# Kernel tuning notes

Measured on AMD Instinct MI355X. Metric: run time of the kernel, lower is better.

The kernel has to match this reference:

```python
import jax, jax.numpy as jnp
import numpy as np

N_NODES = 100000
N_EDGES = 1600000
IN_DIM, HID_DIM, OUT_DIM = 256, 128, 64


def gcn_conv(x, row, col, w, W, b, n):
    # PyG GCNConv (eval): add self-loops (weight 1), symmetric normalization,
    # linear transform, scatter-add aggregation at target nodes.
    row = jnp.concatenate([row, jnp.arange(n, dtype=row.dtype)])
    col = jnp.concatenate([col, jnp.arange(n, dtype=col.dtype)])
    w = jnp.concatenate([w, jnp.ones((n,), dtype=w.dtype)])
    deg = jax.ops.segment_sum(w, col, num_segments=n)  # [N]
    dinv = jnp.where(deg > 0, jax.lax.rsqrt(deg), 0.0)
    norm = dinv[row] * w * dinv[col]  # [E+N]
    h = x @ W  # [N, out]
    msg = norm[:, None] * h[row]  # gather: [E+N, out]
    out = jax.ops.segment_sum(msg, col, num_segments=n)  # scatter-add
    return out + b


def setup_inputs() -> dict:
    key = jax.random.key(0)
    k = jax.random.split(key, 8)
    x = jax.random.normal(k[0], (N_NODES, IN_DIM), dtype=jnp.float32)
    edge_index = jax.random.randint(k[1], (2, N_EDGES), 0, N_NODES, dtype=jnp.int64)
    edge_weight = jax.random.uniform(k[2], (N_EDGES,), dtype=jnp.float32)
    s1 = 1.0 / np.sqrt(IN_DIM)
    s2 = 1.0 / np.sqrt(HID_DIM)
    W1 = jax.random.uniform(k[3], (IN_DIM, HID_DIM), minval=-s1, maxval=s1, dtype=jnp.float32)
    b1 = jnp.zeros((HID_DIM,), dtype=jnp.float32)
    W2 = jax.random.uniform(k[4], (HID_DIM, OUT_DIM), minval=-s2, maxval=s2, dtype=jnp.float32)
    b2 = jnp.zeros((OUT_DIM,), dtype=jnp.float32)
    return {"x": x, "edge_index": edge_index, "edge_weight": edge_weight,
            "W1": W1, "b1": b1, "W2": W2, "b2": b2}


def reference(x, edge_index, edge_weight, W1, b1, W2, b2):
    row, col = edge_index[0], edge_index[1]
    n = x.shape[0]
    h = gcn_conv(x, row, col, edge_weight, W1, b1, n)
    h = jax.nn.relu(h)  # dropout is identity in eval mode
    out = gcn_conv(h, row, col, edge_weight, W2, b2, n)
    return out
```

## Files before the change

### kernel.cpp

```cpp
#include <hip/hip_runtime.h>
#include <hip/hip_fp16.h>

#define IN_DIM 256
#define HID_DIM 128
#define OUT_DIM 64

typedef short s8v __attribute__((ext_vector_type(8)));
typedef float f32x4 __attribute__((ext_vector_type(4)));


__device__ __forceinline__ unsigned short bf16_rne(float f) {
    unsigned int u = __float_as_uint(f);
    u += 0x7FFFu + ((u >> 16) & 1u);
    return (unsigned short)(u >> 16);
}
__device__ __forceinline__ float bfbits_to_f(unsigned short h) {
    return __uint_as_float(((unsigned int)h) << 16);
}
__device__ __forceinline__ void cvt_split4(float4 f, uint2& hv, uint2& lv) {
    unsigned short h0 = bf16_rne(f.x), h1 = bf16_rne(f.y);
    unsigned short h2 = bf16_rne(f.z), h3 = bf16_rne(f.w);
    unsigned short l0 = bf16_rne(f.x - bfbits_to_f(h0));
    unsigned short l1 = bf16_rne(f.y - bfbits_to_f(h1));
    unsigned short l2 = bf16_rne(f.z - bfbits_to_f(h2));
    unsigned short l3 = bf16_rne(f.w - bfbits_to_f(h3));
    hv.x = (unsigned int)h0 | ((unsigned int)h1 << 16);
    hv.y = (unsigned int)h2 | ((unsigned int)h3 << 16);
    lv.x = (unsigned int)l0 | ((unsigned int)l1 << 16);
    lv.y = (unsigned int)l2 | ((unsigned int)l3 << 16);
}

__global__ __launch_bounds__(256) void wsplit_kernel(const float* __restrict__ W,
        unsigned short* __restrict__ wth, unsigned short* __restrict__ wtl,
        int K, int NCOL) {
    int idx = blockIdx.x * 256 + threadIdx.x;
    if (idx < K * NCOL) {
        int k = idx / NCOL, nn = idx % NCOL;
        float f = W[idx];
        unsigned short h = bf16_rne(f);
        unsigned short l = bf16_rne(f - bfbits_to_f(h));
        wth[nn * K + k] = h;
        wtl[nn * K + k] = l;
    }
}


#define FPSCALE 16777216.0f
#define FPMASK  ((1ULL << 40) - 1)

__global__ __launch_bounds__(256) void init_kernel(unsigned long long* packed, int n) {
    int i = blockIdx.x * 256 + threadIdx.x;
    if (i < n) packed[i] = (1ULL << 24);
}

__global__ __launch_bounds__(256) void deg_cnt_kernel(const int* __restrict__ col,
        const float* __restrict__ w, unsigned long long* packed, int e) {
    int i = blockIdx.x * 256 + threadIdx.x;
    if (i < e) {
        unsigned long long v = (1ULL << 40) |
            (unsigned long long)(w[i] * FPSCALE + 0.5f);
        atomicAdd(&packed[col[i]], v);
    }
}

__global__ __launch_bounds__(256) void dinv_kernel(const unsigned long long* __restrict__ packed,
        float* __restrict__ dinv, int* __restrict__ cnt, int n) {
    int i = blockIdx.x * 256 + threadIdx.x;
    if (i < n) {
        unsigned long long p = packed[i];
        float d = (float)(p & FPMASK) * (1.0f / FPSCALE);
        dinv[i] = d > 0.0f ? rsqrtf(d) : 0.0f;
        cnt[i] = (int)(p >> 40);
    }
}


__global__ __launch_bounds__(256) void scan1_kernel(const int* __restrict__ cnt,
        int* __restrict__ bsum, int n) {
    int t = threadIdx.x;
    int base = blockIdx.x * 1024 + t * 4;
    int s = 0;
    if (base + 3 < n) {
        int4 v = *(const int4*)(cnt + base);
        s = v.x + v.y + v.z + v.w;
    } else {
        for (int i = 0; i < 4; i++) if (base + i < n) s += cnt[base + i];
    }
    __shared__ int sm[256];
    sm[t] = s;
    __syncthreads();
    for (int d = 1; d < 256; d <<= 1) {
        int v = (t >= d) ? sm[t - d] : 0;
        __syncthreads();
        sm[t] += v;
        __syncthreads();
    }
    if (t == 255) bsum[blockIdx.x] = sm[255];
}

__global__ __launch_bounds__(1024) void scan2_kernel(int* bsum, int* total_out, int nb) {
    __shared__ int sm[1024];
    int t = threadIdx.x;
    int v = (t < nb) ? bsum[t] : 0;
    sm[t] = v;
    __syncthreads();
    for (int d = 1; d < 1024; d <<= 1) {
        int u = (t >= d) ? sm[t - d] : 0;
        __syncthreads();
        sm[t] += u;
        __syncthreads();
    }
    int ex = (t == 0) ? 0 : sm[t - 1];
    if (t < nb) bsum[t] = ex;
    if (t == nb - 1) *total_out = sm[t];
}

__global__ __launch_bounds__(256) void scan3_kernel(const int* __restrict__ cnt,
        const int* __restrict__ bsum, int* __restrict__ offsets,
        int* __restrict__ cursors, int n) {
    int t = threadIdx.x;
    int base = blockIdx.x * 1024 + t * 4;
    int a[4] = {0, 0, 0, 0};
    if (base + 3 < n) {
        int4 v = *(const int4*)(cnt + base);
        a[0] = v.x; a[1] = v.y; a[2] = v.z; a[3] = v.w;
    } else {
        for (int i = 0; i < 4; i++) if (base + i < n) a[i] = cnt[base + i];
    }
    int s = a[0] + a[1] + a[2] + a[3];
    __shared__ int sm[256];
    sm[t] = s;
    __syncthreads();
    for (int d = 1; d < 256; d <<= 1) {
        int u = (t >= d) ? sm[t - d] : 0;
        __syncthreads();
        sm[t] += u;
        __syncthreads();
    }
    int pre = bsum[blockIdx.x] + ((t == 0) ? 0 : sm[t - 1]);
    int o0 = pre, o1 = o0 + a[0], o2 = o1 + a[1], o3 = o2 + a[2];
    if (base + 3 < n) {
        *(int4*)(offsets + base) = make_int4(o0, o1, o2, o3);
        *(int4*)(cursors + base) = make_int4(o0, o1, o2, o3);
    } else {
        int o[4] = {o0, o1, o2, o3};
        for (int i = 0; i < 4; i++) if (base + i < n) {
            offsets[base + i] = o[i];
            cursors[base + i] = o[i];
        }
    }
}

__global__ __launch_bounds__(256) void fill_csc_kernel(const int* __restrict__ row,
        const int* __restrict__ col, const float* __restrict__ w,
        const float* __restrict__ dinv, int* cursors,
        int2* __restrict__ csc, int e) {
    int i = blockIdx.x * 256 + threadIdx.x;
    if (i < e) {
        int r = row[i], c = col[i];
        float nrm = dinv[r] * w[i] * dinv[c];
        int p = atomicAdd(&cursors[c], 1);
        csc[p] = make_int2(r, __float_as_int(nrm));
    }
}


template<int K, int NCOL>
__global__ __launch_bounds__(256) void gemm_mfma_kernel(
        const float* __restrict__ x, const unsigned short* __restrict__ wth,
        const unsigned short* __restrict__ wtl, __half* __restrict__ out, int n) {
    constexpr int NT = NCOL / 16;
    constexpr int NCH = K / 32;
    __shared__ unsigned short sAh[128 * 40];
    __shared__ unsigned short sAl[128 * 40];
    __shared__ unsigned short sBh[NCOL * 40];
    __shared__ unsigned short sBl[NCOL * 40];

    int t = threadIdx.x;
    int wave = t >> 6, lane = t & 63, quad = lane >> 4, r16 = lane & 15;
    long rowBase = (long)blockIdx.x * 128;

    f32x4 acc[2][NT];
#pragma unroll
    for (int mi = 0; mi < 2; mi++)
#pragma unroll
        for (int nt = 0; nt < NT; nt++) acc[mi][nt] = (f32x4)0.0f;

    int srow = t >> 1;
    int skseg = (t & 1) * 16;
    long sgr = rowBase + srow; if (sgr > n - 1) sgr = n - 1;
    const float* xrow = x + sgr * K + skseg;

    for (int kc = 0; kc < NCH; kc++) {
        const float4* xs = (const float4*)(xrow + kc * 32);
        float4 f0 = xs[0], f1 = xs[1], f2 = xs[2], f3 = xs[3];
        uint2 h0, l0, h1, l1, h2, l2, h3, l3;
        cvt_split4(f0, h0, l0); cvt_split4(f1, h1, l1);
        cvt_split4(f2, h2, l2); cvt_split4(f3, h3, l3);
        *(uint4*)(sAh + srow * 40 + skseg)     = make_uint4(h0.x, h0.y, h1.x, h1.y);
        *(uint4*)(sAh + srow * 40 + skseg + 8) = make_uint4(h2.x, h2.y, h3.x, h3.y);
        *(uint4*)(sAl + srow * 40 + skseg)     = make_uint4(l0.x, l0.y, l1.x, l1.y);
        *(uint4*)(sAl + srow * 40 + skseg + 8) = make_uint4(l2.x, l2.y, l3.x, l3.y);
        for (int c = t; c < NCOL * 4; c += 256) {
            int nn = c >> 2, ks = (c & 3) * 8;
            *(uint4*)(sBh + nn * 40 + ks) = *(const uint4*)(wth + nn * K + kc * 32 + ks);
            *(uint4*)(sBl + nn * 40 + ks) = *(const uint4*)(wtl + nn * K + kc * 32 + ks);
        }
        __syncthreads();
        const unsigned short* pa  = sAh + (wave * 32 + r16) * 40 + quad * 8;
        const unsigned short* pal = sAl + (wave * 32 + r16) * 40 + quad * 8;
        s8v ah0 = *(const s8v*)pa;
        s8v ah1 = *(const s8v*)(pa + 16 * 40);
        s8v al0 = *(const s8v*)pal;
        s8v al1 = *(const s8v*)(pal + 16 * 40);
#pragma unroll
        for (int nt = 0; nt < NT; nt++) {
            const unsigned short* pb  = sBh + (nt * 16 + r16) * 40 + quad * 8;
            const unsigned short* pbl = sBl + (nt * 16 + r16) * 40 + quad * 8;
            s8v bh = *(const s8v*)pb;
            s8v bl = *(const s8v*)pbl;
            acc[0][nt] = __builtin_amdgcn_mfma_f32_16x16x32_bf16(ah0, bh, acc[0][nt], 0, 0, 0);
            acc[0][nt] = __builtin_amdgcn_mfma_f32_16x16x32_bf16(al0, bh, acc[0][nt], 0, 0, 0);
            acc[0][nt] = __builtin_amdgcn_mfma_f32_16x16x32_bf16(ah0, bl, acc[0][nt], 0, 0, 0);
            acc[1][nt] = __builtin_amdgcn_mfma_f32_16x16x32_bf16(ah1, bh, acc[1][nt], 0, 0, 0);
            acc[1][nt] = __builtin_amdgcn_mfma_f32_16x16x32_bf16(al1, bh, acc[1][nt], 0, 0, 0);
            acc[1][nt] = __builtin_amdgcn_mfma_f32_16x16x32_bf16(ah1, bl, acc[1][nt], 0, 0, 0);
        }
        __syncthreads();
    }
#pragma unroll
    for (int mi = 0; mi < 2; mi++) {
        long gr0 = rowBase + wave * 32 + mi * 16 + quad * 4;
#pragma unroll
        for (int nt = 0; nt < NT; nt++) {
            f32x4 d = acc[mi][nt];
#pragma unroll
            for (int i = 0; i < 4; i++) {
                long gr = gr0 + i;
                if (gr < n) out[gr * NCOL + nt * 16 + r16] = __float2half(d[i]);
            }
        }
    }
}


__device__ __forceinline__ void acc8(float* a, uint4 raw, float w) {
    __half2* hp = (__half2*)&raw;
    float2 f0 = __half22float2(hp[0]);
    float2 f1 = __half22float2(hp[1]);
    float2 f2 = __half22float2(hp[2]);
    float2 f3 = __half22float2(hp[3]);
    a[0] += w * f0.x; a[1] += w * f0.y; a[2] += w * f1.x; a[3] += w * f1.y;
    a[4] += w * f2.x; a[5] += w * f2.y; a[6] += w * f3.x; a[7] += w * f3.y;
}

__device__ __forceinline__ void acc4h(float* a, uint2 raw, float w) {
    __half2* hp = (__half2*)&raw;
    float2 f0 = __half22float2(hp[0]);
    float2 f1 = __half22float2(hp[1]);
    a[0] += w * f0.x; a[1] += w * f0.y; a[2] += w * f1.x; a[3] += w * f1.y;
}


__global__ __launch_bounds__(256) void agg1_kernel(const __half* __restrict__ h,
        const float* __restrict__ dinv, const int* __restrict__ offsets,
        const int2* __restrict__ csc, const float* __restrict__ b,
        float* __restrict__ out, int n) {
    int t = threadIdx.x;
    int lane = t & 63;
    int strm = lane >> 4;
    int li = lane & 15;
    int node = blockIdx.x * 4 + (t >> 6);
    if (node >= n) return;

    float a0[8] = {0,0,0,0,0,0,0,0};
    float a1[8] = {0,0,0,0,0,0,0,0};
    int s = offsets[node], e = offsets[node + 1];

    if (strm == 0) {
        float di = dinv[node];
        uint4 raw = ((const uint4*)(h + (long)node * HID_DIM))[li];
        acc8(a0, raw, di * di);
    }

    int p = s + strm;
    for (; p + 4 < e; p += 8) {
        int2 e0 = csc[p], e1 = csc[p + 4];
        uint4 r0 = ((const uint4*)(h + (long)e0.x * HID_DIM))[li];
        uint4 r1 = ((const uint4*)(h + (long)e1.x * HID_DIM))[li];
        acc8(a0, r0, __int_as_float(e0.y));
        acc8(a1, r1, __int_as_float(e1.y));
    }
    if (p < e) {
        int2 e0 = csc[p];
        uint4 r0 = ((const uint4*)(h + (long)e0.x * HID_DIM))[li];
        acc8(a0, r0, __int_as_float(e0.y));
    }
#pragma unroll
    for (int j = 0; j < 8; j++) a0[j] += a1[j];
#pragma unroll
    for (int j = 0; j < 8; j++) a0[j] += __shfl_down(a0[j], 32);
#pragma unroll
    for (int j = 0; j < 8; j++) a0[j] += __shfl_down(a0[j], 16);
    if (strm == 0) {
        float4 bv0 = ((const float4*)b)[li * 2];
        float4 bv1 = ((const float4*)b)[li * 2 + 1];
        float4 o0 = make_float4(fmaxf(a0[0] + bv0.x, 0.f), fmaxf(a0[1] + bv0.y, 0.f),
                                fmaxf(a0[2] + bv0.z, 0.f), fmaxf(a0[3] + bv0.w, 0.f));
        float4 o1 = make_float4(fmaxf(a0[4] + bv1.x, 0.f), fmaxf(a0[5] + bv1.y, 0.f),
                                fmaxf(a0[6] + bv1.z, 0.f), fmaxf(a0[7] + bv1.w, 0.f));
        float4* dst = (float4*)(out + (long)node * HID_DIM);
        dst[li * 2] = o0;
        dst[li * 2 + 1] = o1;
    }
}


__global__ __launch_bounds__(256) void agg2_kernel(const __half* __restrict__ h,
        const float* __restrict__ dinv, const int* __restrict__ offsets,
        const int2* __restrict__ csc, const float* __restrict__ b,
        float* __restrict__ out, int n) {
    int t = threadIdx.x;
    int lane = t & 63;
    int strm = lane >> 4;
    int li = lane & 15;
    int node = blockIdx.x * 4 + (t >> 6);
    if (node >= n) return;

    float a0[4] = {0,0,0,0};
    float a1[4] = {0,0,0,0};
    int s = offsets[node], e = offsets[node + 1];

    if (strm == 0) {
        float di = dinv[node];
        uint2 raw = ((const uint2*)(h + (long)node * OUT_DIM))[li];
        acc4h(a0, raw, di * di);
    }

    int p = s + strm;
    for (; p + 4 < e; p += 8) {
        int2 e0 = csc[p], e1 = csc[p + 4];
        uint2 r0 = ((const uint2*)(h + (long)e0.x * OUT_DIM))[li];
        uint2 r1 = ((const uint2*)(h + (long)e1.x * OUT_DIM))[li];
        acc4h(a0, r0, __int_as_float(e0.y));
        acc4h(a1, r1, __int_as_float(e1.y));
    }
    if (p < e) {
        int2 e0 = csc[p];
        uint2 r0 = ((const uint2*)(h + (long)e0.x * OUT_DIM))[li];
        acc4h(a0, r0, __int_as_float(e0.y));
    }
#pragma unroll
    for (int j = 0; j < 4; j++) a0[j] += a1[j];
#pragma unroll
    for (int j = 0; j < 4; j++) a0[j] += __shfl_down(a0[j], 32);
#pragma unroll
    for (int j = 0; j < 4; j++) a0[j] += __shfl_down(a0[j], 16);
    if (strm == 0) {
        float4 bv = ((const float4*)b)[li];
        ((float4*)(out + (long)node * OUT_DIM))[li] =
            make_float4(a0[0] + bv.x, a0[1] + bv.y, a0[2] + bv.z, a0[3] + bv.w);
    }
}


extern "C" void kernel_launch(void* const* d_in, const int* in_sizes, int n_in,
                              void* d_out, int out_size, void* d_ws, size_t ws_size,
                              hipStream_t stream) {
    const float* x  = (const float*)d_in[0];
    const int*   ei = (const int*)d_in[1];
    const float* w  = (const float*)d_in[2];
    const float* W1 = (const float*)d_in[3];
    const float* b1 = (const float*)d_in[4];
    const float* W2 = (const float*)d_in[5];
    const float* b2 = (const float*)d_in[6];
    float* out = (float*)d_out;

    int N = in_sizes[0] / IN_DIM;
    int E = in_sizes[2];
    const int* row = ei;
    const int* col = ei + E;

    char* base = (char*)d_ws;
    size_t off = 0;
    auto alloc = [&](size_t bytes) -> void* {
        void* p = base + off;
        off += (bytes + 255) & ~(size_t)255;
        return p;
    };
    unsigned long long* packed = (unsigned long long*)alloc((size_t)N * 8);
    float* dinv     = (float*)alloc((size_t)N * 4);
    int*   cnt      = (int*)  alloc((size_t)N * 4);
    int*   offsets  = (int*)  alloc((size_t)(N + 1) * 4);
    int*   cursors  = (int*)  alloc((size_t)N * 4);
    int*   bsum     = (int*)  alloc((size_t)1024 * 4);
    int2*  csc      = (int2*) alloc((size_t)E * 8);
    __half* h       = (__half*)alloc((size_t)N * HID_DIM * 2);
    float* hagg     = (float*)alloc((size_t)N * HID_DIM * 4);
    unsigned short* wt1h = (unsigned short*)alloc((size_t)IN_DIM * HID_DIM * 2);
    unsigned short* wt1l = (unsigned short*)alloc((size_t)IN_DIM * HID_DIM * 2);
    unsigned short* wt2h = (unsigned short*)alloc((size_t)HID_DIM * OUT_DIM * 2);
    unsigned short* wt2l = (unsigned short*)alloc((size_t)HID_DIM * OUT_DIM * 2);

    int gN = (N + 255) / 256;
    int gE = (E + 255) / 256;
    int gGemm = (N + 127) / 128;
    int gAgg = (N + 3) / 4;
    int nbScan = (N + 1023) / 1024;

    wsplit_kernel<<<(IN_DIM * HID_DIM + 255) / 256, 256, 0, stream>>>(
        W1, wt1h, wt1l, IN_DIM, HID_DIM);
    wsplit_kernel<<<(HID_DIM * OUT_DIM + 255) / 256, 256, 0, stream>>>(
        W2, wt2h, wt2l, HID_DIM, OUT_DIM);
    init_kernel<<<gN, 256, 0, stream>>>(packed, N);
    deg_cnt_kernel<<<gE, 256, 0, stream>>>(col, w, packed, E);
    dinv_kernel<<<gN, 256, 0, stream>>>(packed, dinv, cnt, N);
    scan1_kernel<<<nbScan, 256, 0, stream>>>(cnt, bsum, N);
    scan2_kernel<<<1, 1024, 0, stream>>>(bsum, offsets + N, nbScan);
    scan3_kernel<<<nbScan, 256, 0, stream>>>(cnt, bsum, offsets, cursors, N);
    fill_csc_kernel<<<gE, 256, 0, stream>>>(row, col, w, dinv, cursors, csc, E);
    gemm_mfma_kernel<IN_DIM, HID_DIM><<<gGemm, 256, 0, stream>>>(x, wt1h, wt1l, h, N);
    agg1_kernel<<<gAgg, 256, 0, stream>>>(h, dinv, offsets, csc, b1, hagg, N);
    gemm_mfma_kernel<HID_DIM, OUT_DIM><<<gGemm, 256, 0, stream>>>(hagg, wt2h, wt2l, h, N);
    agg2_kernel<<<gAgg, 256, 0, stream>>>(h, dinv, offsets, csc, b2, out, N);
}
```

Before: 493.8 us.

## Use atomic return slot for CSC fill and fold dinv into GEMM epilogue

The degree-count atomic now returns the old packed value, and its count field gives each edge a local slot. The CSC fill becomes offsets[c]+slot with no second atomic pass or cursor array. The symmetric normalisation is refactored: rows of h are pre-scaled by dinv[src] in the GEMM epilogue, and the aggregation multiplies by dinv[dst] at the end. As a result the CSC stores the raw edge weight, and the fill kernel no longer does two random dinv gathers. The cost is an extra E-sized int array written and read, plus a dinv load per output row in the GEMM.

```diff
diff --git a/kernel.cpp b/kernel.cpp
--- a/kernel.cpp
+++ b/kernel.cpp
@@ -54,12 +54,14 @@
 }
 
 __global__ __launch_bounds__(256) void deg_cnt_kernel(const int* __restrict__ col,
-        const float* __restrict__ w, unsigned long long* packed, int e) {
+        const float* __restrict__ w, unsigned long long* packed,
+        int* __restrict__ arr, int e) {
     int i = blockIdx.x * 256 + threadIdx.x;
     if (i < e) {
         unsigned long long v = (1ULL << 40) |
             (unsigned long long)(w[i] * FPSCALE + 0.5f);
-        atomicAdd(&packed[col[i]], v);
+        unsigned long long old = atomicAdd(&packed[col[i]], v);
+        arr[i] = (int)(old >> 40);
     }
 }
 
@@ -116,8 +118,7 @@
 }
 
 __global__ __launch_bounds__(256) void scan3_kernel(const int* __restrict__ cnt,
-        const int* __restrict__ bsum, int* __restrict__ offsets,
-        int* __restrict__ cursors, int n) {
+        const int* __restrict__ bsum, int* __restrict__ offsets, int n) {
     int t = threadIdx.x;
     int base = blockIdx.x * 1024 + t * 4;
     int a[4] = {0, 0, 0, 0};
@@ -141,26 +142,22 @@
     int o0 = pre, o1 = o0 + a[0], o2 = o1 + a[1], o3 = o2 + a[2];
     if (base + 3 < n) {
         *(int4*)(offsets + base) = make_int4(o0, o1, o2, o3);
-        *(int4*)(cursors + base) = make_int4(o0, o1, o2, o3);
     } else {
         int o[4] = {o0, o1, o2, o3};
-        for (int i = 0; i < 4; i++) if (base + i < n) {
-            offsets[base + i] = o[i];
-            cursors[base + i] = o[i];
-        }
-    }
-}
+        for (int i = 0; i < 4; i++) if (base + i < n) offsets[base + i] = o[i];
+    }
+}
+
 
 __global__ __launch_bounds__(256) void fill_csc_kernel(const int* __restrict__ row,
         const int* __restrict__ col, const float* __restrict__ w,
-        const float* __restrict__ dinv, int* cursors,
+        const int* __restrict__ offsets, const int* __restrict__ arr,
         int2* __restrict__ csc, int e) {
     int i = blockIdx.x * 256 + threadIdx.x;
     if (i < e) {
-        int r = row[i], c = col[i];
-        float nrm = dinv[r] * w[i] * dinv[c];
-        int p = atomicAdd(&cursors[c], 1);
-        csc[p] = make_int2(r, __float_as_int(nrm));
+        int c = col[i];
+        int p = offsets[c] + arr[i];
+        csc[p] = make_int2(row[i], __float_as_int(w[i]));
     }
 }
 
@@ -168,7 +165,8 @@
 template<int K, int NCOL>
 __global__ __launch_bounds__(256) void gemm_mfma_kernel(
         const float* __restrict__ x, const unsigned short* __restrict__ wth,
-        const unsigned short* __restrict__ wtl, __half* __restrict__ out, int n) {
+        const unsigned short* __restrict__ wtl, const float* __restrict__ dinv,
+        __half* __restrict__ out, int n) {
     constexpr int NT = NCOL / 16;
     constexpr int NCH = K / 32;
     __shared__ unsigned short sAh[128 * 40];
@@ -237,7 +235,8 @@
 #pragma unroll
             for (int i = 0; i < 4; i++) {
                 long gr = gr0 + i;
-                if (gr < n) out[gr * NCOL + nt * 16 + r16] = __float2half(d[i]);
+                if (gr < n) out[gr * NCOL + nt * 16 + r16] =
+                    __float2half(d[i] * dinv[gr]);
             }
         }
     }
@@ -278,9 +277,8 @@
     int s = offsets[node], e = offsets[node + 1];
 
     if (strm == 0) {
-        float di = dinv[node];
         uint4 raw = ((const uint4*)(h + (long)node * HID_DIM))[li];
-        acc8(a0, raw, di * di);
+        acc8(a0, raw, 1.0f);
     }
 
     int p = s + strm;
@@ -303,12 +301,13 @@
 #pragma unroll
     for (int j = 0; j < 8; j++) a0[j] += __shfl_down(a0[j], 16);
     if (strm == 0) {
+        float di = dinv[node];
         float4 bv0 = ((const float4*)b)[li * 2];
         float4 bv1 = ((const float4*)b)[li * 2 + 1];
-        float4 o0 = make_float4(fmaxf(a0[0] + bv0.x, 0.f), fmaxf(a0[1] + bv0.y, 0.f),
-                                fmaxf(a0[2] + bv0.z, 0.f), fmaxf(a0[3] + bv0.w, 0.f));
-        float4 o1 = make_float4(fmaxf(a0[4] + bv1.x, 0.f), fmaxf(a0[5] + bv1.y, 0.f),
-                                fmaxf(a0[6] + bv1.z, 0.f), fmaxf(a0[7] + bv1.w, 0.f));
+        float4 o0 = make_float4(fmaxf(di * a0[0] + bv0.x, 0.f), fmaxf(di * a0[1] + bv0.y, 0.f),
+                                fmaxf(di * a0[2] + bv0.z, 0.f), fmaxf(di * a0[3] + bv0.w, 0.f));
+        float4 o1 = make_float4(fmaxf(di * a0[4] + bv1.x, 0.f), fmaxf(di * a0[5] + bv1.y, 0.f),
+                                fmaxf(di * a0[6] + bv1.z, 0.f), fmaxf(di * a0[7] + bv1.w, 0.f));
         float4* dst = (float4*)(out + (long)node * HID_DIM);
         dst[li * 2] = o0;
         dst[li * 2 + 1] = o1;
@@ -332,9 +331,8 @@
     int s = offsets[node], e = offsets[node + 1];
 
     if (strm == 0) {
-        float di = dinv[node];
         uint2 raw = ((const uint2*)(h + (long)node * OUT_DIM))[li];
-        acc4h(a0, raw, di * di);
+        acc4h(a0, raw, 1.0f);
     }
 
     int p = s + strm;
@@ -357,9 +355,11 @@
 #pragma unroll
     for (int j = 0; j < 4; j++) a0[j] += __shfl_down(a0[j], 16);
     if (strm == 0) {
+        float di = dinv[node];
         float4 bv = ((const float4*)b)[li];
         ((float4*)(out + (long)node * OUT_DIM))[li] =
-            make_float4(a0[0] + bv.x, a0[1] + bv.y, a0[2] + bv.z, a0[3] + bv.w);
+            make_float4(di * a0[0] + bv.x, di * a0[1] + bv.y,
+                        di * a0[2] + bv.z, di * a0[3] + bv.w);
     }
 }
 
@@ -392,7 +392,7 @@
     float* dinv     = (float*)alloc((size_t)N * 4);
     int*   cnt      = (int*)  alloc((size_t)N * 4);
     int*   offsets  = (int*)  alloc((size_t)(N + 1) * 4);
-    int*   cursors  = (int*)  alloc((size_t)N * 4);
+    int*   arr      = (int*)  alloc((size_t)E * 4);
     int*   bsum     = (int*)  alloc((size_t)1024 * 4);
     int2*  csc      = (int2*) alloc((size_t)E * 8);
     __half* h       = (__half*)alloc((size_t)N * HID_DIM * 2);
@@ -413,14 +413,14 @@
     wsplit_kernel<<<(HID_DIM * OUT_DIM + 255) / 256, 256, 0, stream>>>(
         W2, wt2h, wt2l, HID_DIM, OUT_DIM);
     init_kernel<<<gN, 256, 0, stream>>>(packed, N);
-    deg_cnt_kernel<<<gE, 256, 0, stream>>>(col, w, packed, E);
+    deg_cnt_kernel<<<gE, 256, 0, stream>>>(col, w, packed, arr, E);
     dinv_kernel<<<gN, 256, 0, stream>>>(packed, dinv, cnt, N);
     scan1_kernel<<<nbScan, 256, 0, stream>>>(cnt, bsum, N);
     scan2_kernel<<<1, 1024, 0, stream>>>(bsum, offsets + N, nbScan);
-    scan3_kernel<<<nbScan, 256, 0, stream>>>(cnt, bsum, offsets, cursors, N);
-    fill_csc_kernel<<<gE, 256, 0, stream>>>(row, col, w, dinv, cursors, csc, E);
-    gemm_mfma_kernel<IN_DIM, HID_DIM><<<gGemm, 256, 0, stream>>>(x, wt1h, wt1l, h, N);
+    scan3_kernel<<<nbScan, 256, 0, stream>>>(cnt, bsum, offsets, N);
+    fill_csc_kernel<<<gE, 256, 0, stream>>>(row, col, w, offsets, arr, csc, E);
+    gemm_mfma_kernel<IN_DIM, HID_DIM><<<gGemm, 256, 0, stream>>>(x, wt1h, wt1l, dinv, h, N);
     agg1_kernel<<<gAgg, 256, 0, stream>>>(h, dinv, offsets, csc, b1, hagg, N);
-    gemm_mfma_kernel<HID_DIM, OUT_DIM><<<gGemm, 256, 0, stream>>>(hagg, wt2h, wt2l, h, N);
+    gemm_mfma_kernel<HID_DIM, OUT_DIM><<<gGemm, 256, 0, stream>>>(hagg, wt2h, wt2l, dinv, h, N);
     agg2_kernel<<<gAgg, 256, 0, stream>>>(h, dinv, offsets, csc, b2, out, N);
 }
```

New measurement: 474.6 us. -3.9%, faster.
